# Performance work log

Measured on AMD Instinct MI355X. Metric: run time of the kernel, lower is better.

Reference implementation:

```python
import jax, jax.numpy as jnp
import numpy as np

B, S, HID = 2, 1024, 2048
H, HK, D = 32, 4, 128
G = H // HK
EPS = 1e-6
SCALE = 1.0 / np.sqrt(D)
ROPE_THETA = 1000000.0


def _rope_tables(seq_len, dim, theta):
    inv_freq = 1.0 / (theta ** (np.arange(0, dim, 2, dtype=np.float32) / dim))
    t = np.arange(seq_len, dtype=np.float32)
    freqs = np.outer(t, inv_freq)                      # [S, D/2]
    emb = np.concatenate([freqs, freqs], axis=-1)       # [S, D]
    return (jnp.asarray(np.cos(emb))[None, :, None, :],
            jnp.asarray(np.sin(emb))[None, :, None, :])  # [1,S,1,D]


def setup_inputs() -> dict:
    key = jax.random.key(0)
    k1, k2, k3 = jax.random.split(key, 3)
    cos, sin = _rope_tables(S, D, ROPE_THETA)
    return {
        "hidden_states": jax.random.normal(k1, (B, S, HID), jnp.float32),
        "cos": cos,
        "sin": sin,
        "w_qkv": jax.random.normal(k2, (HID, (H + 2 * HK) * D), jnp.float32) * 0.02,
        "q_norm_w": jnp.ones((D,), jnp.float32),
        "k_norm_w": jnp.ones((D,), jnp.float32),
        "w_o": jax.random.normal(k3, (H * D, HID), jnp.float32) * 0.02,
    }


def _rms_norm(x, w):
    xf = x.astype(jnp.float32)
    var = jnp.mean(xf * xf, axis=-1, keepdims=True)
    return (w * (xf * jax.lax.rsqrt(var + EPS))).astype(x.dtype)


def _rotate_half(x):
    x1, x2 = jnp.split(x, 2, axis=-1)
    return jnp.concatenate([-x2, x1], axis=-1)


def reference(hidden_states, cos, sin, w_qkv, q_norm_w, k_norm_w, w_o):
    b, s, _ = hidden_states.shape
    qkv = hidden_states @ w_qkv                          # [B,S,(H+2HK)*D]
    q, k, v = jnp.split(qkv, [H * D, (H + HK) * D], axis=-1)
    q = q.reshape(b, s, H, D)
    k = k.reshape(b, s, HK, D)
    v = v.reshape(b, s, HK, D)
    # per-head RMSNorm on q/k, then rotary (BSH layout)
    q = _rms_norm(q, q_norm_w)
    k = _rms_norm(k, k_norm_w)
    q = q * cos + _rotate_half(q) * sin
    k = k * cos + _rotate_half(k) * sin
    # grouped-query causal SDPA (prefill path, sparse_mode=2)
    qg = q.reshape(b, s, HK, G, D)
    scores = jnp.einsum("bqkgd,bskd->bkgqs", qg, k) * SCALE  # [B,HK,G,S,S]
    causal = jnp.tril(jnp.ones((s, s), bool))
    scores = jnp.where(causal, scores, jnp.finfo(scores.dtype).min)
    probs = jax.nn.softmax(scores, axis=-1)
    ctx = jnp.einsum("bkgqs,bskd->bqkgd", probs, v)          # [B,S,HK,G,D]
    ctx = ctx.reshape(b, s, H * D)
    return ctx @ w_o                                          # [B,S,HID]
```

## Files before the change

kernel.cpp:

```cpp
#include <hip/hip_runtime.h>

#define B_   2
#define S_   1024
#define HID_ 2048
#define H_   32
#define HK_  4
#define D_   128
#define NQKV ((H_ + 2 * HK_) * D_)
#define TOK  (B_ * S_)

typedef short bf16x8  __attribute__((ext_vector_type(8)));
typedef short short4v __attribute__((ext_vector_type(4)));
typedef float f32x4   __attribute__((ext_vector_type(4)));
typedef int   i32x4   __attribute__((ext_vector_type(4)));

__device__ inline short f2bf(float f) {
  unsigned u = __builtin_bit_cast(unsigned, f);
  u += 0x7fffu + ((u >> 16) & 1u);
  return (short)(u >> 16);
}

__device__ __forceinline__ void gld_lds16(const short* g, short* l) {
  __builtin_amdgcn_global_load_lds((__attribute__((address_space(1))) void*)g,
                                   (__attribute__((address_space(3))) void*)l, 16, 0, 0);
}

__global__ __launch_bounds__(256) void cast_f32_bf16(const float* __restrict__ in,
                                                     short* __restrict__ out, int n4) {
  int i = blockIdx.x * 256 + threadIdx.x;
  if (i >= n4) return;
  f32x4 v = ((const f32x4*)in)[i];
  short4v o;
  o[0] = f2bf(v[0]); o[1] = f2bf(v[1]); o[2] = f2bf(v[2]); o[3] = f2bf(v[3]);
  ((short4v*)out)[i] = o;
}

__global__ __launch_bounds__(256) void transpose_cast(const float* __restrict__ in,
                                                      short* __restrict__ out,
                                                      int K, int N) {
  __shared__ float tile[32][33];
  int nb = blockIdx.x * 32, kb = blockIdx.y * 32;
  int c = threadIdx.x & 31, r0 = threadIdx.x >> 5;
#pragma unroll
  for (int i = 0; i < 4; i++) {
    int r = r0 + i * 8;
    tile[r][c] = in[(size_t)(kb + r) * N + nb + c];
  }
  __syncthreads();
#pragma unroll
  for (int i = 0; i < 4; i++) {
    int r = r0 + i * 8;
    out[(size_t)(nb + r) * K + kb + c] = f2bf(tile[c][r]);
  }
}

__global__ __launch_bounds__(256) void gemm_bt128(const short* __restrict__ A,
                                                  const short* __restrict__ Bt,
                                                  float* __restrict__ C,
                                                  int M, int N, int Kfull, int klen) {
  const int tid  = threadIdx.x;
  const int m0   = blockIdx.y * 128;
  const int n0   = blockIdx.x * 128;
  const int kz0  = blockIdx.z * klen;
  const int w    = tid >> 6, lane = tid & 63;
  const int quad = lane >> 4, l16 = lane & 15;
  const int wm   = (w >> 1) * 64, wn = (w & 1) * 64;

  __shared__ short As[128 * 64];
  __shared__ short Bs[128 * 64];

  const f32x4 z = {0.f, 0.f, 0.f, 0.f};
  f32x4 acc[4][4];
#pragma unroll
  for (int i = 0; i < 4; i++)
#pragma unroll
    for (int j = 0; j < 4; j++) acc[i][j] = z;

  const int srow = lane >> 3;
  const int lc   = (lane & 7) ^ srow;

  for (int kk = 0; kk < klen; kk += 64) {
    const int k0 = kz0 + kk;
#pragma unroll
    for (int i = 0; i < 4; i++) {
      int rb = w * 32 + i * 8;
      gld_lds16(&A [(size_t)(m0 + rb + srow) * Kfull + k0 + lc * 8], &As[rb * 64]);
      gld_lds16(&Bt[(size_t)(n0 + rb + srow) * Kfull + k0 + lc * 8], &Bs[rb * 64]);
    }
    __syncthreads();
#pragma unroll
    for (int kb = 0; kb < 2; kb++) {
      const int pc = ((kb * 4 + quad) ^ (l16 & 7)) * 8;
      bf16x8 a[4], b[4];
#pragma unroll
      for (int f = 0; f < 4; f++) {
        a[f] = *(const bf16x8*)&As[(wm + f * 16 + l16) * 64 + pc];
        b[f] = *(const bf16x8*)&Bs[(wn + f * 16 + l16) * 64 + pc];
      }
#pragma unroll
      for (int fi = 0; fi < 4; fi++)
#pragma unroll
        for (int fj = 0; fj < 4; fj++)
          acc[fi][fj] = __builtin_amdgcn_mfma_f32_16x16x32_bf16(a[fi], b[fj], acc[fi][fj], 0, 0, 0);
    }
    __syncthreads();
  }

  float* Cz = C + (size_t)blockIdx.z * M * N;
#pragma unroll
  for (int fi = 0; fi < 4; fi++) {
    int row0 = m0 + wm + fi * 16 + quad * 4;
#pragma unroll
    for (int fj = 0; fj < 4; fj++) {
      int col = n0 + wn + fj * 16 + l16;
#pragma unroll
      for (int r = 0; r < 4; r++)
        Cz[(size_t)(row0 + r) * N + col] = acc[fi][fj][r];
    }
  }
}

__global__ __launch_bounds__(256) void add2(const float* __restrict__ a,
                                            const float* __restrict__ b,
                                            float* __restrict__ c, int n4) {
  int i = blockIdx.x * 256 + threadIdx.x;
  if (i >= n4) return;
  f32x4 va = ((const f32x4*)a)[i], vb = ((const f32x4*)b)[i];
  ((f32x4*)c)[i] = va + vb;
}

__global__ __launch_bounds__(64) void rmsnorm_rope_qk(const float* __restrict__ qkv,
                                                      const float* __restrict__ cosT,
                                                      const float* __restrict__ sinT,
                                                      const float* __restrict__ qw,
                                                      const float* __restrict__ kw,
                                                      short* __restrict__ Qb,
                                                      short* __restrict__ Kb) {
  int t    = blockIdx.x;
  int hd   = blockIdx.y;
  int b    = t >> 10;
  int s    = t & (S_ - 1);
  int lane = threadIdx.x;
  const float QSC = 0.08838834764831845f * 1.4426950408889634f;
  const float* base;
  const float* w;
  short* dst;
  float osc;
  if (hd < H_) {
    base = qkv + (size_t)t * NQKV + hd * D_;
    w = qw; osc = QSC;
    dst = Qb + (((size_t)b * H_ + hd) * S_ + s) * D_;
  } else {
    base = qkv + (size_t)t * NQKV + H_ * D_ + (hd - H_) * D_;
    w = kw; osc = 1.0f;
    dst = Kb + (((size_t)b * HK_ + (hd - H_)) * S_ + s) * D_;
  }
  float x1 = base[lane], x2 = base[lane + 64];
  float ss = x1 * x1 + x2 * x2;
#pragma unroll
  for (int off = 32; off > 0; off >>= 1) ss += __shfl_xor(ss, off, 64);
  float rn = rsqrtf(ss * (1.0f / 128.0f) + 1e-6f);
  float y1 = x1 * rn * w[lane], y2 = x2 * rn * w[lane + 64];
  float c1 = cosT[s * D_ + lane],      s1 = sinT[s * D_ + lane];
  float c2 = cosT[s * D_ + lane + 64], s2 = sinT[s * D_ + lane + 64];
  dst[lane]      = f2bf((y1 * c1 - y2 * s1) * osc);
  dst[lane + 64] = f2bf((y2 * c2 + y1 * s2) * osc);
}

__global__ __launch_bounds__(256) void v_pack(const float* __restrict__ qkv,
                                              short* __restrict__ Vt) {
  int bk = blockIdx.x;
  int s0 = blockIdx.y * 64;
  int d  = threadIdx.x & 127;
  int sg = threadIdx.x >> 7;
  int b = bk >> 2, kh = bk & 3;
  short buf[32];
  const float* src = qkv + ((size_t)(b * S_ + s0 + sg * 32)) * NQKV + (H_ + HK_) * D_ + kh * D_ + d;
#pragma unroll
  for (int sj = 0; sj < 32; sj++)
    buf[sj] = f2bf(src[(size_t)sj * NQKV]);
  short* dst = Vt + ((size_t)bk * D_ + d) * S_ + s0 + sg * 32;
#pragma unroll
  for (int i = 0; i < 4; i++) ((i32x4*)dst)[i] = ((const i32x4*)buf)[i];
}

__global__ __launch_bounds__(256) void attn_mfma5(const short* __restrict__ Qb,
                                                  const short* __restrict__ Kb,
                                                  const short* __restrict__ Vt,
                                                  short* __restrict__ ctx) {
  const int qmap[8] = {7, 0, 6, 1, 5, 2, 4, 3};
  const int qt = qmap[blockIdx.x & 7];
  const int h  = blockIdx.y;
  const int b  = blockIdx.z;
  const int kh = h >> 3;
  const int q0 = qt * 128;
  const int tid = threadIdx.x, w = tid >> 6, lane = tid & 63;
  const int quad = lane >> 4, l16 = lane & 15;
  const float MBIAS = 18.0f;

  __shared__ short Ks[128 * 64];
  __shared__ short Vs[144 * 64];
  __shared__ short Ps[4][2][16 * 72];

  for (int i = tid; i < 16 * 64; i += 256) Vs[128 * 64 + i] = (short)0x3F80;

  const short* Qbase = Qb + (((size_t)b * H_ + h) * S_ + q0) * D_;
  bf16x8 aq[2][4];
#pragma unroll
  for (int fi = 0; fi < 2; fi++)
#pragma unroll
    for (int kb = 0; kb < 4; kb++)
      aq[fi][kb] = *(const bf16x8*)&Qbase[(size_t)(fi * 64 + w * 16 + l16) * D_ + kb * 32 + quad * 8];

  const f32x4 z = {0.f, 0.f, 0.f, 0.f};
  f32x4 O[2][9];
#pragma unroll
  for (int fi = 0; fi < 2; fi++)
#pragma unroll
    for (int n = 0; n < 9; n++) O[fi][n] = z;

  const short* Kbase = Kb + ((size_t)(b * HK_ + kh) * S_) * D_;
  const short* Vbase = Vt + ((size_t)(b * HK_ + kh) * D_) * S_;

  const int srow = lane >> 3;
  const int lc   = (lane & 7) ^ srow;

  const int nkt = 2 * qt + 2;
  for (int kt = 0; kt < nkt; kt++) {
    const int k0 = kt * 64;
    __syncthreads();
#pragma unroll
    for (int i = 0; i < 4; i++) {
      int rb = w * 32 + i * 8;
      int rr = rb + srow;
      gld_lds16(&Kbase[(size_t)(k0 + (rr & 63)) * D_ + (rr >> 6) * 64 + lc * 8], &Ks[rb * 64]);
      gld_lds16(&Vbase[(size_t)rr * S_ + k0 + lc * 8], &Vs[rb * 64]);
    }
    __syncthreads();

#pragma unroll
    for (int nb = 0; nb < 4; nb++) {
      f32x4 s0 = z, s1 = z;
#pragma unroll
      for (int kb = 0; kb < 4; kb++) {
        const int c  = kb * 4 + quad;
        const int c7 = c & 7;
        const int rr = (c >> 3) * 64 + nb * 16 + l16;
        bf16x8 bk = *(const bf16x8*)&Ks[rr * 64 + (c7 ^ (l16 & 7)) * 8];
        s0 = __builtin_amdgcn_mfma_f32_16x16x32_bf16(aq[0][kb], bk, s0, 0, 0, 0);
        s1 = __builtin_amdgcn_mfma_f32_16x16x32_bf16(aq[1][kb], bk, s1, 0, 0, 0);
      }
      const int col = k0 + nb * 16 + l16;
#pragma unroll
      for (int r = 0; r < 4; r++) {
        int row0 = q0 + w * 16 + quad * 4 + r;
        float p0 = (col > row0) ? 0.0f : exp2f(s0[r] - MBIAS);
        float p1 = (col > row0 + 64) ? 0.0f : exp2f(s1[r] - MBIAS);
        Ps[w][0][(quad * 4 + r) * 72 + nb * 16 + l16] = f2bf(p0);
        Ps[w][1][(quad * 4 + r) * 72 + nb * 16 + l16] = f2bf(p1);
      }
    }

#pragma unroll
    for (int kb2 = 0; kb2 < 2; kb2++) {
      bf16x8 ap0 = *(const bf16x8*)&Ps[w][0][l16 * 72 + kb2 * 32 + quad * 8];
      bf16x8 ap1 = *(const bf16x8*)&Ps[w][1][l16 * 72 + kb2 * 32 + quad * 8];
      const int c7 = kb2 * 4 + quad;
#pragma unroll
      for (int nb2 = 0; nb2 < 9; nb2++) {
        int d = nb2 * 16 + l16;
        bf16x8 bv = *(const bf16x8*)&Vs[d * 64 + (c7 ^ (d & 7)) * 8];
        O[0][nb2] = __builtin_amdgcn_mfma_f32_16x16x32_bf16(ap0, bv, O[0][nb2], 0, 0, 0);
        O[1][nb2] = __builtin_amdgcn_mfma_f32_16x16x32_bf16(ap1, bv, O[1][nb2], 0, 0, 0);
      }
    }
  }

#pragma unroll
  for (int fi = 0; fi < 2; fi++)
#pragma unroll
    for (int r = 0; r < 4; r++) {
      float inv = 1.0f / O[fi][8][r];
      size_t row = (size_t)(b * S_ + q0 + fi * 64 + w * 16 + quad * 4 + r);
      short* dst = ctx + row * (H_ * D_) + h * D_;
#pragma unroll
      for (int nb2 = 0; nb2 < 8; nb2++)
        dst[nb2 * 16 + l16] = f2bf(O[fi][nb2][r] * inv);
    }
}

extern "C" void kernel_launch(void* const* d_in, const int* in_sizes, int n_in,
                              void* d_out, int out_size, void* d_ws, size_t ws_size,
                              hipStream_t stream) {
  (void)in_sizes; (void)n_in; (void)out_size; (void)ws_size;
  const float* hidden = (const float*)d_in[0];
  const float* cosT   = (const float*)d_in[1];
  const float* sinT   = (const float*)d_in[2];
  const float* wqkv   = (const float*)d_in[3];
  const float* qnw    = (const float*)d_in[4];
  const float* knw    = (const float*)d_in[5];
  const float* wo     = (const float*)d_in[6];
  float* out = (float*)d_out;

  char* ws = (char*)d_ws;
  float* qkv = (float*)(ws);
  short* hb  = (short*)(ws + 41943040);
  short* wT  = (short*)(ws + 41943040 + 8388608);
  short* ctx = (short*)(ws + 41943040 + 8388608 + 20971520);
  short* Kb  = hb;
  short* Vt  = hb + 1048576;
  short* Qb  = wT;
  float* part = (float*)ws;

  cast_f32_bf16<<<4096, 256, 0, stream>>>(hidden, hb, TOK * HID_ / 4);
  transpose_cast<<<dim3(NQKV / 32, HID_ / 32), 256, 0, stream>>>(wqkv, wT, HID_, NQKV);
  gemm_bt128<<<dim3(NQKV / 128, TOK / 128, 1), 256, 0, stream>>>(hb, wT, qkv, TOK, NQKV, HID_, HID_);
  rmsnorm_rope_qk<<<dim3(TOK, H_ + HK_), 64, 0, stream>>>(qkv, cosT, sinT, qnw, knw, Qb, Kb);
  v_pack<<<dim3(B_ * HK_, S_ / 64), 256, 0, stream>>>(qkv, Vt);
  attn_mfma5<<<dim3(S_ / 128, H_, B_), 256, 0, stream>>>(Qb, Kb, Vt, ctx);
  transpose_cast<<<dim3(HID_ / 32, (H_ * D_) / 32), 256, 0, stream>>>(wo, wT, H_ * D_, HID_);
  gemm_bt128<<<dim3(HID_ / 128, TOK / 128, 2), 256, 0, stream>>>(ctx, wT, part, TOK, HID_, H_ * D_, (H_ * D_) / 2);
  add2<<<(TOK * HID_ / 4 + 255) / 256, 256, 0, stream>>>(part, part + (size_t)TOK * HID_, out, TOK * HID_ / 4);
}
```

Baseline: 348.4 us.

## Fuse RMSNorm, RoPE and V packing into the QKV GEMM epilogue

Adds a specialised QKV GEMM whose epilogue does per-head RMSNorm and rotary on Q/K tiles and writes transposed bf16 V directly. The 128-wide N tile matches one head, so row sums of squares are reduced across lanes and between paired waves through shared memory, and the rotate-half partner half is exchanged via the reused A/B tile buffers. This removes the fp32 qkv round trip through global memory and two extra kernel launches. In exchange the epilogue does scattered 2-byte stores and uncoalesced cos/sin loads, and the Q/K partner values pass through bf16 before the rotation.

```diff
diff --git a/kernel.cpp b/kernel.cpp
--- a/kernel.cpp
+++ b/kernel.cpp
@@ -18,6 +18,9 @@
   unsigned u = __builtin_bit_cast(unsigned, f);
   u += 0x7fffu + ((u >> 16) & 1u);
   return (short)(u >> 16);
+}
+__device__ inline float bf2f(short s) {
+  return __builtin_bit_cast(float, ((unsigned)(unsigned short)s) << 16);
 }
 
 __device__ __forceinline__ void gld_lds16(const short* g, short* l) {
@@ -129,59 +132,152 @@
   ((f32x4*)c)[i] = va + vb;
 }
 
-__global__ __launch_bounds__(64) void rmsnorm_rope_qk(const float* __restrict__ qkv,
-                                                      const float* __restrict__ cosT,
-                                                      const float* __restrict__ sinT,
-                                                      const float* __restrict__ qw,
-                                                      const float* __restrict__ kw,
-                                                      short* __restrict__ Qb,
-                                                      short* __restrict__ Kb) {
-  int t    = blockIdx.x;
-  int hd   = blockIdx.y;
-  int b    = t >> 10;
-  int s    = t & (S_ - 1);
-  int lane = threadIdx.x;
-  const float QSC = 0.08838834764831845f * 1.4426950408889634f;
-  const float* base;
-  const float* w;
-  short* dst;
-  float osc;
-  if (hd < H_) {
-    base = qkv + (size_t)t * NQKV + hd * D_;
-    w = qw; osc = QSC;
-    dst = Qb + (((size_t)b * H_ + hd) * S_ + s) * D_;
-  } else {
-    base = qkv + (size_t)t * NQKV + H_ * D_ + (hd - H_) * D_;
-    w = kw; osc = 1.0f;
-    dst = Kb + (((size_t)b * HK_ + (hd - H_)) * S_ + s) * D_;
-  }
-  float x1 = base[lane], x2 = base[lane + 64];
-  float ss = x1 * x1 + x2 * x2;
-#pragma unroll
-  for (int off = 32; off > 0; off >>= 1) ss += __shfl_xor(ss, off, 64);
-  float rn = rsqrtf(ss * (1.0f / 128.0f) + 1e-6f);
-  float y1 = x1 * rn * w[lane], y2 = x2 * rn * w[lane + 64];
-  float c1 = cosT[s * D_ + lane],      s1 = sinT[s * D_ + lane];
-  float c2 = cosT[s * D_ + lane + 64], s2 = sinT[s * D_ + lane + 64];
-  dst[lane]      = f2bf((y1 * c1 - y2 * s1) * osc);
-  dst[lane + 64] = f2bf((y2 * c2 + y1 * s2) * osc);
-}
-
-__global__ __launch_bounds__(256) void v_pack(const float* __restrict__ qkv,
-                                              short* __restrict__ Vt) {
-  int bk = blockIdx.x;
-  int s0 = blockIdx.y * 64;
-  int d  = threadIdx.x & 127;
-  int sg = threadIdx.x >> 7;
-  int b = bk >> 2, kh = bk & 3;
-  short buf[32];
-  const float* src = qkv + ((size_t)(b * S_ + s0 + sg * 32)) * NQKV + (H_ + HK_) * D_ + kh * D_ + d;
-#pragma unroll
-  for (int sj = 0; sj < 32; sj++)
-    buf[sj] = f2bf(src[(size_t)sj * NQKV]);
-  short* dst = Vt + ((size_t)bk * D_ + d) * S_ + s0 + sg * 32;
-#pragma unroll
-  for (int i = 0; i < 4; i++) ((i32x4*)dst)[i] = ((const i32x4*)buf)[i];
+__global__ __launch_bounds__(256) void gemm_qkv(const short* __restrict__ A,
+                                                const short* __restrict__ Bt,
+                                                const float* __restrict__ cosT,
+                                                const float* __restrict__ sinT,
+                                                const float* __restrict__ qw,
+                                                const float* __restrict__ kw,
+                                                short* __restrict__ Qb,
+                                                short* __restrict__ Kb,
+                                                short* __restrict__ Vt) {
+  const int tid  = threadIdx.x;
+  const int m0   = blockIdx.y * 128;
+  const int n0   = blockIdx.x * 128;
+  const int w    = tid >> 6, lane = tid & 63;
+  const int quad = lane >> 4, l16 = lane & 15;
+  const int wm   = (w >> 1) * 64, wn = (w & 1) * 64;
+
+  __shared__ short As[128 * 64];
+  __shared__ short Bs[128 * 64];
+  __shared__ float ss_lds[4][64];
+
+  const f32x4 z = {0.f, 0.f, 0.f, 0.f};
+  f32x4 acc[4][4];
+#pragma unroll
+  for (int i = 0; i < 4; i++)
+#pragma unroll
+    for (int j = 0; j < 4; j++) acc[i][j] = z;
+
+  const int srow = lane >> 3;
+  const int lc   = (lane & 7) ^ srow;
+
+  for (int k0 = 0; k0 < HID_; k0 += 64) {
+#pragma unroll
+    for (int i = 0; i < 4; i++) {
+      int rb = w * 32 + i * 8;
+      gld_lds16(&A [(size_t)(m0 + rb + srow) * HID_ + k0 + lc * 8], &As[rb * 64]);
+      gld_lds16(&Bt[(size_t)(n0 + rb + srow) * HID_ + k0 + lc * 8], &Bs[rb * 64]);
+    }
+    __syncthreads();
+#pragma unroll
+    for (int kb = 0; kb < 2; kb++) {
+      const int pc = ((kb * 4 + quad) ^ (l16 & 7)) * 8;
+      bf16x8 a[4], b[4];
+#pragma unroll
+      for (int f = 0; f < 4; f++) {
+        a[f] = *(const bf16x8*)&As[(wm + f * 16 + l16) * 64 + pc];
+        b[f] = *(const bf16x8*)&Bs[(wn + f * 16 + l16) * 64 + pc];
+      }
+#pragma unroll
+      for (int fi = 0; fi < 4; fi++)
+#pragma unroll
+        for (int fj = 0; fj < 4; fj++)
+          acc[fi][fj] = __builtin_amdgcn_mfma_f32_16x16x32_bf16(a[fi], b[fj], acc[fi][fj], 0, 0, 0);
+    }
+    __syncthreads();
+  }
+
+  const int hd = n0 >> 7;
+  const int bb = m0 >> 10;
+  const int sW = (m0 & (S_ - 1)) + wm;
+
+  if (hd >= H_ + HK_) {
+    const int khv = hd - (H_ + HK_);
+    short* dstV = Vt + ((size_t)(bb * HK_ + khv) * D_) * S_;
+#pragma unroll
+    for (int fi = 0; fi < 4; fi++) {
+      int s = sW + fi * 16 + quad * 4;
+#pragma unroll
+      for (int fj = 0; fj < 4; fj++) {
+        int d = wn + fj * 16 + l16;
+        short4v o;
+#pragma unroll
+        for (int r = 0; r < 4; r++) o[r] = f2bf(acc[fi][fj][r]);
+        *(short4v*)&dstV[(size_t)d * S_ + s] = o;
+      }
+    }
+    return;
+  }
+
+  float ssp[4][4];
+#pragma unroll
+  for (int fi = 0; fi < 4; fi++)
+#pragma unroll
+    for (int r = 0; r < 4; r++) {
+      float t = 0.f;
+#pragma unroll
+      for (int fj = 0; fj < 4; fj++) t += acc[fi][fj][r] * acc[fi][fj][r];
+      ssp[fi][r] = t;
+    }
+#pragma unroll
+  for (int off = 1; off < 16; off <<= 1)
+#pragma unroll
+    for (int fi = 0; fi < 4; fi++)
+#pragma unroll
+      for (int r = 0; r < 4; r++) ssp[fi][r] += __shfl_xor(ssp[fi][r], off, 64);
+  if (l16 == 0)
+#pragma unroll
+    for (int fi = 0; fi < 4; fi++)
+#pragma unroll
+      for (int r = 0; r < 4; r++) ss_lds[w][fi * 16 + quad * 4 + r] = ssp[fi][r];
+  __syncthreads();
+  float rn[4][4];
+#pragma unroll
+  for (int fi = 0; fi < 4; fi++)
+#pragma unroll
+    for (int r = 0; r < 4; r++) {
+      int row = fi * 16 + quad * 4 + r;
+      rn[fi][r] = rsqrtf((ss_lds[w][row] + ss_lds[w ^ 1][row]) * (1.0f / 128.0f) + 1e-6f);
+    }
+  const float* wv = (hd < H_) ? qw : kw;
+  float wgt[4];
+#pragma unroll
+  for (int fj = 0; fj < 4; fj++) wgt[fj] = wv[wn + fj * 16 + l16];
+
+  short* xown = (w & 1) ? &Bs[(w >> 1) * 4096] : &As[(w >> 1) * 4096];
+  short* xpar = (w & 1) ? &As[(w >> 1) * 4096] : &Bs[(w >> 1) * 4096];
+#pragma unroll
+  for (int fi = 0; fi < 4; fi++)
+#pragma unroll
+    for (int fj = 0; fj < 4; fj++) {
+      short4v y4;
+#pragma unroll
+      for (int r = 0; r < 4; r++) y4[r] = f2bf(acc[fi][fj][r] * rn[fi][r] * wgt[fj]);
+      *(short4v*)&xown[(((fi * 4 + fj) * 4 + quad) * 16 + l16) * 4] = y4;
+    }
+  __syncthreads();
+
+  const float sign = (wn == 0) ? -1.0f : 1.0f;
+  const float osc  = (hd < H_) ? (0.08838834764831845f * 1.4426950408889634f) : 1.0f;
+  short* dstQ = (hd < H_) ? (Qb + (((size_t)bb * H_ + hd) * S_) * D_)
+                          : (Kb + (((size_t)bb * HK_ + (hd - H_)) * S_) * D_);
+#pragma unroll
+  for (int fi = 0; fi < 4; fi++)
+#pragma unroll
+    for (int fj = 0; fj < 4; fj++) {
+      short4v yp4 = *(const short4v*)&xpar[(((fi * 4 + fj) * 4 + quad) * 16 + l16) * 4];
+      int d = wn + fj * 16 + l16;
+#pragma unroll
+      for (int r = 0; r < 4; r++) {
+        int s = sW + fi * 16 + quad * 4 + r;
+        float y  = acc[fi][fj][r] * rn[fi][r] * wgt[fj];
+        float yp = bf2f(yp4[r]);
+        float c  = cosT[s * D_ + d];
+        float sn = sinT[s * D_ + d];
+        dstQ[(size_t)s * D_ + d] = f2bf((y * c + sign * yp * sn) * osc);
+      }
+    }
 }
 
 __global__ __launch_bounds__(256) void attn_mfma5(const short* __restrict__ Qb,
@@ -303,20 +399,17 @@
   float* out = (float*)d_out;
 
   char* ws = (char*)d_ws;
-  float* qkv = (float*)(ws);
+  short* Qb  = (short*)ws;
+  short* Kb  = (short*)(ws + 16777216);
+  short* Vt  = (short*)(ws + 16777216 + 2097152);
   short* hb  = (short*)(ws + 41943040);
   short* wT  = (short*)(ws + 41943040 + 8388608);
   short* ctx = (short*)(ws + 41943040 + 8388608 + 20971520);
-  short* Kb  = hb;
-  short* Vt  = hb + 1048576;
-  short* Qb  = wT;
   float* part = (float*)ws;
 
   cast_f32_bf16<<<4096, 256, 0, stream>>>(hidden, hb, TOK * HID_ / 4);
   transpose_cast<<<dim3(NQKV / 32, HID_ / 32), 256, 0, stream>>>(wqkv, wT, HID_, NQKV);
-  gemm_bt128<<<dim3(NQKV / 128, TOK / 128, 1), 256, 0, stream>>>(hb, wT, qkv, TOK, NQKV, HID_, HID_);
-  rmsnorm_rope_qk<<<dim3(TOK, H_ + HK_), 64, 0, stream>>>(qkv, cosT, sinT, qnw, knw, Qb, Kb);
-  v_pack<<<dim3(B_ * HK_, S_ / 64), 256, 0, stream>>>(qkv, Vt);
+  gemm_qkv<<<dim3(NQKV / 128, TOK / 128), 256, 0, stream>>>(hb, wT, cosT, sinT, qnw, knw, Qb, Kb, Vt);
   attn_mfma5<<<dim3(S_ / 128, H_, B_), 256, 0, stream>>>(Qb, Kb, Vt, ctx);
   transpose_cast<<<dim3(HID_ / 32, (H_ * D_) / 32), 256, 0, stream>>>(wo, wT, H_ * D_, HID_);
   gemm_bt128<<<dim3(HID_ / 128, TOK / 128, 2), 256, 0, stream>>>(ctx, wT, part, TOK, HID_, H_ * D_, (H_ * D_) / 2);
```

After: 330.9 us. 5.0% less time.
